# Optimization experiments

Measured on AMD Instinct MI355X. Metric: run time of the kernel, lower is better.

Reference implementation:

```python
import jax, jax.numpy as jnp
import numpy as np

EMBED_DIM = 1024
NUM_HEADS = 16
HEAD_DIM = EMBED_DIM // NUM_HEADS
B, T = 2, 2048


def setup_inputs() -> dict:
    key = jax.random.key(0)
    ks = jax.random.split(key, 9)
    s = 1.0 / np.sqrt(EMBED_DIM)
    return {
        "x": jax.random.normal(ks[0], (B, T, EMBED_DIM), dtype=jnp.float32),
        "W_q": jax.random.uniform(ks[1], (EMBED_DIM, EMBED_DIM), jnp.float32, -s, s),
        "b_q": jax.random.uniform(ks[2], (EMBED_DIM,), jnp.float32, -s, s),
        "W_k": jax.random.uniform(ks[3], (EMBED_DIM, EMBED_DIM), jnp.float32, -s, s),
        "b_k": jax.random.uniform(ks[4], (EMBED_DIM,), jnp.float32, -s, s),
        "W_v": jax.random.uniform(ks[5], (EMBED_DIM, EMBED_DIM), jnp.float32, -s, s),
        "b_v": jax.random.uniform(ks[6], (EMBED_DIM,), jnp.float32, -s, s),
        "W_o": jax.random.uniform(ks[7], (EMBED_DIM, EMBED_DIM), jnp.float32, -s, s),
        "b_o": jax.random.uniform(ks[8], (EMBED_DIM,), jnp.float32, -s, s),
    }


def reference(x, W_q, b_q, W_k, b_k, W_v, b_v, W_o, b_o):
    Bv, Tv, C = x.shape
    # QKV projections (torch Linear: x @ W.T + b); split into heads -> (B,H,T,Dh)
    def proj(W, b):
        return (x @ W.T + b).reshape(Bv, Tv, NUM_HEADS, HEAD_DIM).transpose(0, 2, 1, 3)
    q, k, v = proj(W_q, b_q), proj(W_k, b_k), proj(W_v, b_v)
    scale = 1.0 / np.sqrt(HEAD_DIM).astype(np.float32)
    scores = jnp.einsum("bhqd,bhkd->bhqk", q, k) * scale  # (B,H,T,T)
    causal = jnp.tril(jnp.ones((Tv, Tv), dtype=bool))
    scores = jnp.where(causal, scores, -jnp.inf)
    attn = jax.nn.softmax(scores, axis=-1)
    # dropout is identity in eval / p=0
    out = jnp.einsum("bhqk,bhkd->bhqd", attn, v)  # (B,H,T,Dh)
    out = out.transpose(0, 2, 1, 3).reshape(Bv, Tv, C)
    return out @ W_o.T + b_o
```

## Files before the change

kernel.cpp:

```cpp
#include <hip/hip_runtime.h>
#include <hip/hip_bf16.h>


typedef __bf16 bf16;
typedef __attribute__((ext_vector_type(8))) __bf16 bf16x8;
typedef __attribute__((ext_vector_type(4))) __bf16 bf16x4;
typedef __attribute__((ext_vector_type(4))) float floatx4;

#define LOG2E 1.44269504088896340736f

__device__ __forceinline__ void gl2lds16(const void* g, void* l) {
  __builtin_amdgcn_global_load_lds((const __attribute__((address_space(1))) void*)g,
                                   (__attribute__((address_space(3))) void*)l, 16, 0, 0);
}

__global__ __launch_bounds__(256) void cast_all(
    const float* __restrict__ x, const float* __restrict__ wq,
    const float* __restrict__ wk, const float* __restrict__ wv,
    const float* __restrict__ wo, bf16* __restrict__ dst)
{
  const size_t M1 = (size_t)1 << 20;
  size_t i4 = ((size_t)blockIdx.x * 256 + threadIdx.x) * 4;
  const float* src = x;
  size_t off = i4;
  if (i4 >= 4 * M1) {
    size_t r = i4 - 4 * M1;
    int seg = (int)(r >> 20);
    off = r & (M1 - 1);
    src = (seg == 0) ? wq : (seg == 1) ? wk : (seg == 2) ? wv : wo;
  }
  float4 f = *(const float4*)(src + off);
  bf16x4 o = { (bf16)f.x, (bf16)f.y, (bf16)f.z, (bf16)f.w };
  *(bf16x4*)(dst + i4) = o;
}

template<bool F32OUT, bool QKV, int BN>
__global__ __launch_bounds__(256, 3) void gemm_bt(
    const bf16* __restrict__ A, const bf16* __restrict__ Wb,
    const float* __restrict__ bq, const float* __restrict__ bk,
    const float* __restrict__ bv, void* __restrict__ outb,
    bf16* __restrict__ vt, int M, int N, int K, float qscale)
{
  __shared__ bf16 As[128 * 64];
  __shared__ bf16 Bs[BN * 64];
  const int tid = threadIdx.x;
  const int lane = tid & 63;
  const int wid = tid >> 6;
  const int l15 = lane & 15, l4 = lane >> 4;
  constexpr int I = (BN == 128) ? 4 : 2;
  const int wr = (BN == 128) ? (wid >> 1) : wid;
  const int wc = (BN == 128) ? (wid & 1) : 0;

  const bf16* W;
  const float* bias;
  float osc = 1.0f;
  int n0, mat = 0;
  bf16* outh;
  float* outf;
  if (QKV) {
    mat = blockIdx.x >> 3;
    n0 = (blockIdx.x & 7) << 7;
    W = Wb + ((size_t)mat << 20);
    bias = (mat == 0) ? bq : (mat == 1 ? bk : bv);
    if (mat == 0) osc = qscale;
    outh = (bf16*)outb + ((size_t)mat << 22);
    outf = nullptr;
  } else {
    n0 = blockIdx.x * BN;
    W = Wb;
    bias = bq;
    outf = (float*)outb;
    outh = nullptr;
  }
  const int m0 = blockIdx.y << 7;

  floatx4 acc[I][4] = {};

  for (int k0 = 0; k0 < K; k0 += 64) {
#pragma unroll
    for (int it = 0; it < 4; ++it) {
      int c = it * 256 + tid;
      int row = c >> 3, gs = ((c & 7) ^ (row & 7)) << 3;
      gl2lds16(A + (size_t)(m0 + row) * K + k0 + gs, As + c * 8);
    }
#pragma unroll
    for (int it = 0; it < BN / 32; ++it) {
      int c = it * 256 + tid;
      int row = c >> 3, gs = ((c & 7) ^ (row & 7)) << 3;
      gl2lds16(W + (size_t)(n0 + row) * K + k0 + gs, Bs + c * 8);
    }
    __syncthreads();
#pragma unroll
    for (int kk = 0; kk < 2; ++kk) {
      bf16x8 af[I], bfr[4];
#pragma unroll
      for (int i = 0; i < I; ++i) {
        int r = wr * (I * 16) + i * 16 + l15;
        int g = (kk * 4 + l4) ^ (r & 7);
        af[i] = *(const bf16x8*)(As + r * 64 + g * 8);
      }
#pragma unroll
      for (int j = 0; j < 4; ++j) {
        int r = wc * 64 + j * 16 + l15;
        int g = (kk * 4 + l4) ^ (r & 7);
        bfr[j] = *(const bf16x8*)(Bs + r * 64 + g * 8);
      }
#pragma unroll
      for (int i = 0; i < I; ++i)
#pragma unroll
        for (int j = 0; j < 4; ++j)
          acc[i][j] = __builtin_amdgcn_mfma_f32_16x16x32_bf16(af[i], bfr[j], acc[i][j], 0, 0, 0);
    }
    __syncthreads();
  }

  if (QKV && mat == 2) {
#pragma unroll
    for (int j = 0; j < 4; ++j) {
      int col = n0 + wc * 64 + j * 16 + l15;
      float bv_ = bias[col];
      int h = col >> 6, d = col & 63;
#pragma unroll
      for (int i = 0; i < I; ++i) {
        int row = m0 + wr * (I * 16) + i * 16 + l4 * 4;
        int bb = row >> 11, t = row & 2047;
        bf16x4 pk;
#pragma unroll
        for (int rg = 0; rg < 4; ++rg) pk[rg] = (bf16)(acc[i][j][rg] + bv_);
        *(bf16x4*)(vt + (((size_t)(bb * 16 + h)) << 17) + ((size_t)d << 11) + t) = pk;
      }
    }
    return;
  }

#pragma unroll
  for (int j = 0; j < 4; ++j) {
    int col = n0 + wc * 64 + j * 16 + l15;
    float bv_ = bias[col];
#pragma unroll
    for (int i = 0; i < I; ++i) {
#pragma unroll
      for (int rg = 0; rg < 4; ++rg) {
        int row = m0 + wr * (I * 16) + i * 16 + l4 * 4 + rg;
        float v = (acc[i][j][rg] + bv_) * osc;
        if (F32OUT) outf[(size_t)row * N + col] = v;
        else        outh[(size_t)row * N + col] = (bf16)v;
      }
    }
  }
}

__global__ __launch_bounds__(256, 2) void attn_kernel(
    const bf16* __restrict__ Q, const bf16* __restrict__ Kg,
    const bf16* __restrict__ Vt, bf16* __restrict__ AO)
{
  constexpr int T = 2048, C = 1024;
  __shared__ bf16 Ks[2][64 * 64];
  __shared__ bf16 Vts[2][64 * 64];
  __shared__ bf16 Ps[4][32 * 68];

  const int tid = threadIdx.x;
  const int lane = tid & 63;
  const int w = tid >> 6;
  const int l15 = lane & 15, l4 = lane >> 4;

  const int u = blockIdx.x;
  const int bh = u & 31;
  const int p = u >> 5;
  const int qt = (p < 8) ? (15 - p) : (p - 8);
  const int q0 = qt << 7;
  const int nkt = 2 * qt + 2;
  const size_t base = ((size_t)(bh >> 4) * T) * C + (bh & 15) * 64;
  const bf16* vtb = Vt + ((size_t)bh << 17);

  auto stageK = [&](int j0, int bufi) {
#pragma unroll
    for (int it = 0; it < 2; ++it) {
      int c = it * 256 + tid;
      int row = c >> 3, s = (c & 7) ^ (row & 7);
      gl2lds16(Kg + base + (size_t)(j0 + row) * C + s * 8, &Ks[bufi][c * 8]);
    }
  };
  auto stageV = [&](int j0, int bufi) {
#pragma unroll
    for (int it = 0; it < 2; ++it) {
      int c = it * 256 + tid;
      int row = c >> 3, s = (c & 7) ^ (row & 7);
      gl2lds16(vtb + ((size_t)row << 11) + j0 + s * 8, &Vts[bufi][c * 8]);
    }
  };

  const int qwave = q0 + w * 32;

  bf16x8 qf[2][2];
#pragma unroll
  for (int tq = 0; tq < 2; ++tq) {
    const bf16* qp = Q + base + (size_t)(qwave + tq * 16 + l15) * C + l4 * 8;
    qf[tq][0] = *(const bf16x8*)(qp);
    qf[tq][1] = *(const bf16x8*)(qp + 32);
  }
  floatx4 o[2][4] = {};
  float mrow[2] = {-1e38f, -1e38f};
  float lrow[2] = {0.f, 0.f};

  stageK(0, 0);
  stageV(0, 0);

  for (int jt = 0; jt < nkt; ++jt) {
    __syncthreads();
    const int cur = jt & 1;
    if (jt + 1 < nkt) {
      stageK((jt + 1) << 6, cur ^ 1);
      stageV((jt + 1) << 6, cur ^ 1);
    }
    const int j0 = jt << 6;
    if (j0 > qwave + 31) continue;

    floatx4 s4[4][2] = {};
#pragma unroll
    for (int kk = 0; kk < 2; ++kk) {
      bf16x8 kf[4];
#pragma unroll
      for (int tj = 0; tj < 4; ++tj) {
        int r = tj * 16 + l15;
        int sl = (kk * 4 + l4) ^ (r & 7);
        kf[tj] = *(const bf16x8*)(&Ks[cur][r * 64 + sl * 8]);
      }
#pragma unroll
      for (int tj = 0; tj < 4; ++tj)
#pragma unroll
        for (int tq = 0; tq < 2; ++tq)
          s4[tj][tq] = __builtin_amdgcn_mfma_f32_16x16x32_bf16(kf[tj], qf[tq][kk], s4[tj][tq], 0, 0, 0);
    }

    if (j0 + 63 > qwave) {
#pragma unroll
      for (int tj = 0; tj < 4; ++tj) {
        int j = j0 + tj * 16 + l4 * 4;
#pragma unroll
        for (int tq = 0; tq < 2; ++tq) {
          int q = qwave + tq * 16 + l15;
#pragma unroll
          for (int rg = 0; rg < 4; ++rg)
            if (j + rg > q) s4[tj][tq][rg] = -3e38f;
        }
      }
    }

    float al[2];
#pragma unroll
    for (int tq = 0; tq < 2; ++tq) {
      float mx = -3e38f;
#pragma unroll
      for (int tj = 0; tj < 4; ++tj)
#pragma unroll
        for (int rg = 0; rg < 4; ++rg)
          mx = fmaxf(mx, s4[tj][tq][rg]);
      mx = fmaxf(mx, __shfl_xor(mx, 16, 64));
      mx = fmaxf(mx, __shfl_xor(mx, 32, 64));
      float mnew = fmaxf(mrow[tq], mx);
      al[tq] = __builtin_amdgcn_exp2f(mrow[tq] - mnew);
      mrow[tq] = mnew;
      float psum = 0.f;
#pragma unroll
      for (int tj = 0; tj < 4; ++tj)
#pragma unroll
        for (int rg = 0; rg < 4; ++rg) {
          float e = __builtin_amdgcn_exp2f(s4[tj][tq][rg] - mnew);
          s4[tj][tq][rg] = e;
          psum += e;
        }
      psum += __shfl_xor(psum, 16, 64);
      psum += __shfl_xor(psum, 32, 64);
      lrow[tq] = lrow[tq] * al[tq] + psum;
    }

#pragma unroll
    for (int tq = 0; tq < 2; ++tq)
#pragma unroll
      for (int tj = 0; tj < 4; ++tj) {
        bf16x4 pk = { (bf16)s4[tj][tq][0], (bf16)s4[tj][tq][1],
                      (bf16)s4[tj][tq][2], (bf16)s4[tj][tq][3] };
        *(bf16x4*)(&Ps[w][(tq * 16 + l15) * 68 + tj * 16 + l4 * 4]) = pk;
      }

#pragma unroll
    for (int tq = 0; tq < 2; ++tq)
#pragma unroll
      for (int td = 0; td < 4; ++td)
#pragma unroll
        for (int rg = 0; rg < 4; ++rg)
          o[tq][td][rg] *= al[tq];

#pragma unroll
    for (int tk = 0; tk < 2; ++tk) {
      bf16x8 pf[2];
#pragma unroll
      for (int tq = 0; tq < 2; ++tq)
        pf[tq] = *(const bf16x8*)(&Ps[w][(tq * 16 + l15) * 68 + tk * 32 + l4 * 8]);
#pragma unroll
      for (int td = 0; td < 4; ++td) {
        int r = td * 16 + l15;
        int sl = (tk * 4 + l4) ^ (r & 7);
        bf16x8 vf = *(const bf16x8*)(&Vts[cur][r * 64 + sl * 8]);
#pragma unroll
        for (int tq = 0; tq < 2; ++tq)
          o[tq][td] = __builtin_amdgcn_mfma_f32_16x16x32_bf16(vf, pf[tq], o[tq][td], 0, 0, 0);
      }
    }
  }

#pragma unroll
  for (int tq = 0; tq < 2; ++tq) {
    float inv = 1.0f / lrow[tq];
    int q = qwave + tq * 16 + l15;
#pragma unroll
    for (int td = 0; td < 4; ++td) {
      bf16x4 ok = { (bf16)(o[tq][td][0] * inv), (bf16)(o[tq][td][1] * inv),
                    (bf16)(o[tq][td][2] * inv), (bf16)(o[tq][td][3] * inv) };
      *(bf16x4*)(AO + base + (size_t)q * C + td * 16 + l4 * 4) = ok;
    }
  }
}

extern "C" void kernel_launch(void* const* d_in, const int* in_sizes, int n_in,
                              void* d_out, int out_size, void* d_ws, size_t ws_size,
                              hipStream_t stream) {
  const float* x  = (const float*)d_in[0];
  const float* Wq = (const float*)d_in[1];
  const float* bq = (const float*)d_in[2];
  const float* Wk = (const float*)d_in[3];
  const float* bk = (const float*)d_in[4];
  const float* Wv = (const float*)d_in[5];
  const float* bv = (const float*)d_in[6];
  const float* Wo = (const float*)d_in[7];
  const float* bo = (const float*)d_in[8];

  bf16* ws = (bf16*)d_ws;
  const size_t M1 = (size_t)1 << 20;
  bf16* xb  = ws;
  bf16* wqb = ws + 4 * M1;
  bf16* wob = ws + 7 * M1;
  bf16* Qp  = ws + 8 * M1;
  bf16* Vtp = ws + 16 * M1;
  bf16* AOp = ws + 20 * M1;

  cast_all<<<8192, 256, 0, stream>>>(x, Wq, Wk, Wv, Wo, ws);
  gemm_bt<false, true, 128><<<dim3(24, 32), 256, 0, stream>>>(
      xb, wqb, bq, bk, bv, (void*)Qp, Vtp, 4096, 1024, 1024, 0.125f * LOG2E);
  attn_kernel<<<512, 256, 0, stream>>>(Qp, Qp + 4 * M1, Vtp, AOp);
  gemm_bt<true, false, 64><<<dim3(16, 32), 256, 0, stream>>>(
      AOp, wob, bo, nullptr, nullptr, d_out, nullptr, 4096, 1024, 1024, 1.0f);
}
```

Measured before the change: 187.7 us.

## Restructure attention into single-wave blocks with 16-key steps and register-resident P

The attention kernel now runs one 64-thread wave per block, each owning 32 query rows, with 2048 blocks instead of 512 four-wave blocks. Keys and values are staged in 16-key chunks, and a waitcnt replaces __syncthreads. P stays in registers and feeds a 16x16x16 MFMA directly, so the LDS round trip for probabilities goes away. Rescaling of O is skipped when the row max did not change. The cost is many more loop iterations with small tiles, higher per-step softmax and shuffle overhead, and less K/V reuse across waves, since each wave now loads its own K/V.

```diff
diff --git a/kernel.cpp b/kernel.cpp
--- a/kernel.cpp
+++ b/kernel.cpp
@@ -6,12 +6,27 @@
 typedef __attribute__((ext_vector_type(8))) __bf16 bf16x8;
 typedef __attribute__((ext_vector_type(4))) __bf16 bf16x4;
 typedef __attribute__((ext_vector_type(4))) float floatx4;
+typedef __attribute__((ext_vector_type(4))) short short4v;
 
 #define LOG2E 1.44269504088896340736f
 
 __device__ __forceinline__ void gl2lds16(const void* g, void* l) {
   __builtin_amdgcn_global_load_lds((const __attribute__((address_space(1))) void*)g,
                                    (__attribute__((address_space(3))) void*)l, 16, 0, 0);
+}
+
+__device__ __forceinline__ floatx4 mfma16(bf16x4 a, bf16x4 b, floatx4 c) {
+#if __has_builtin(__builtin_amdgcn_mfma_f32_16x16x16_bf16)
+  return __builtin_amdgcn_mfma_f32_16x16x16_bf16(a, b, c, 0, 0, 0);
+#elif __has_builtin(__builtin_amdgcn_mfma_f32_16x16x16bf16_1k)
+  return __builtin_amdgcn_mfma_f32_16x16x16bf16_1k(
+      __builtin_bit_cast(short4v, a), __builtin_bit_cast(short4v, b), c, 0, 0, 0);
+#else
+  floatx4 d = c;
+  asm volatile("v_mfma_f32_16x16x16_bf16 %0, %1, %2, %0"
+               : "+v"(d) : "v"(a), "v"(b));
+  return d;
+#endif
 }
 
 __global__ __launch_bounds__(256) void cast_all(
@@ -150,55 +165,51 @@
   }
 }
 
-__global__ __launch_bounds__(256, 2) void attn_kernel(
+__global__ __launch_bounds__(64, 4) void attn_kernel(
     const bf16* __restrict__ Q, const bf16* __restrict__ Kg,
     const bf16* __restrict__ Vt, bf16* __restrict__ AO)
 {
   constexpr int T = 2048, C = 1024;
-  __shared__ bf16 Ks[2][64 * 64];
-  __shared__ bf16 Vts[2][64 * 64];
-  __shared__ bf16 Ps[4][32 * 68];
-
-  const int tid = threadIdx.x;
-  const int lane = tid & 63;
-  const int w = tid >> 6;
+  __shared__ bf16 Ks[2][16 * 64];
+  __shared__ bf16 Vts[2][64 * 16];
+
+  const int lane = threadIdx.x;
   const int l15 = lane & 15, l4 = lane >> 4;
 
   const int u = blockIdx.x;
   const int bh = u & 31;
-  const int p = u >> 5;
-  const int qt = (p < 8) ? (15 - p) : (p - 8);
-  const int q0 = qt << 7;
-  const int nkt = 2 * qt + 2;
+  const int qc = 63 - (u >> 5);
+  const int qw = qc << 5;
+  const int ns = 2 * qc + 2;
   const size_t base = ((size_t)(bh >> 4) * T) * C + (bh & 15) * 64;
   const bf16* vtb = Vt + ((size_t)bh << 17);
 
   auto stageK = [&](int j0, int bufi) {
 #pragma unroll
-    for (int it = 0; it < 2; ++it) {
-      int c = it * 256 + tid;
-      int row = c >> 3, s = (c & 7) ^ (row & 7);
-      gl2lds16(Kg + base + (size_t)(j0 + row) * C + s * 8, &Ks[bufi][c * 8]);
+    for (int i = 0; i < 2; ++i) {
+      int c = i * 64 + lane;
+      int row = c >> 3, g = (c & 7) ^ (row & 7);
+      gl2lds16(Kg + base + (size_t)(j0 + row) * C + g * 8, &Ks[bufi][c * 8]);
     }
   };
   auto stageV = [&](int j0, int bufi) {
 #pragma unroll
-    for (int it = 0; it < 2; ++it) {
-      int c = it * 256 + tid;
-      int row = c >> 3, s = (c & 7) ^ (row & 7);
-      gl2lds16(vtb + ((size_t)row << 11) + j0 + s * 8, &Vts[bufi][c * 8]);
+    for (int i = 0; i < 2; ++i) {
+      int c = i * 64 + lane;
+      int d = c >> 1, h = c & 1;
+      int gh = h ^ ((d >> 2) & 1);
+      gl2lds16(vtb + ((size_t)d << 11) + j0 + gh * 8, &Vts[bufi][c * 8]);
     }
   };
 
-  const int qwave = q0 + w * 32;
-
   bf16x8 qf[2][2];
 #pragma unroll
   for (int tq = 0; tq < 2; ++tq) {
-    const bf16* qp = Q + base + (size_t)(qwave + tq * 16 + l15) * C + l4 * 8;
+    const bf16* qp = Q + base + (size_t)(qw + tq * 16 + l15) * C + l4 * 8;
     qf[tq][0] = *(const bf16x8*)(qp);
     qf[tq][1] = *(const bf16x8*)(qp + 32);
   }
+
   floatx4 o[2][4] = {};
   float mrow[2] = {-1e38f, -1e38f};
   float lrow[2] = {0.f, 0.f};
@@ -206,114 +217,95 @@
   stageK(0, 0);
   stageV(0, 0);
 
-  for (int jt = 0; jt < nkt; ++jt) {
-    __syncthreads();
-    const int cur = jt & 1;
-    if (jt + 1 < nkt) {
-      stageK((jt + 1) << 6, cur ^ 1);
-      stageV((jt + 1) << 6, cur ^ 1);
-    }
-    const int j0 = jt << 6;
-    if (j0 > qwave + 31) continue;
-
-    floatx4 s4[4][2] = {};
+  int buf = 0;
+  for (int s = 0; s < ns; ++s) {
+    __builtin_amdgcn_sched_barrier(0);
+    const bool more = (s + 1 < ns);
+    if (more) {
+      stageK((s + 1) << 4, buf ^ 1);
+      stageV((s + 1) << 4, buf ^ 1);
+      __builtin_amdgcn_s_waitcnt(0x0F74);
+    } else {
+      __builtin_amdgcn_s_waitcnt(0x0F70);
+    }
+    __builtin_amdgcn_sched_barrier(0);
+
+    const int j0 = s << 4;
+
+    floatx4 s4[2] = {};
 #pragma unroll
     for (int kk = 0; kk < 2; ++kk) {
-      bf16x8 kf[4];
-#pragma unroll
-      for (int tj = 0; tj < 4; ++tj) {
-        int r = tj * 16 + l15;
-        int sl = (kk * 4 + l4) ^ (r & 7);
-        kf[tj] = *(const bf16x8*)(&Ks[cur][r * 64 + sl * 8]);
-      }
-#pragma unroll
-      for (int tj = 0; tj < 4; ++tj)
-#pragma unroll
-        for (int tq = 0; tq < 2; ++tq)
-          s4[tj][tq] = __builtin_amdgcn_mfma_f32_16x16x32_bf16(kf[tj], qf[tq][kk], s4[tj][tq], 0, 0, 0);
-    }
-
-    if (j0 + 63 > qwave) {
-#pragma unroll
-      for (int tj = 0; tj < 4; ++tj) {
-        int j = j0 + tj * 16 + l4 * 4;
-#pragma unroll
-        for (int tq = 0; tq < 2; ++tq) {
-          int q = qwave + tq * 16 + l15;
-#pragma unroll
-          for (int rg = 0; rg < 4; ++rg)
-            if (j + rg > q) s4[tj][tq][rg] = -3e38f;
-        }
+      bf16x8 kf = *(const bf16x8*)(&Ks[buf][l15 * 64 + (((kk * 4 + l4) ^ (l15 & 7)) * 8)]);
+      s4[0] = __builtin_amdgcn_mfma_f32_16x16x32_bf16(kf, qf[0][kk], s4[0], 0, 0, 0);
+      s4[1] = __builtin_amdgcn_mfma_f32_16x16x32_bf16(kf, qf[1][kk], s4[1], 0, 0, 0);
+    }
+
+    if (j0 + 15 > qw) {
+      int j = j0 + l4 * 4;
+#pragma unroll
+      for (int tq = 0; tq < 2; ++tq) {
+        int q = qw + tq * 16 + l15;
+#pragma unroll
+        for (int rg = 0; rg < 4; ++rg)
+          if (j + rg > q) s4[tq][rg] = -3e38f;
       }
     }
 
     float al[2];
 #pragma unroll
     for (int tq = 0; tq < 2; ++tq) {
-      float mx = -3e38f;
-#pragma unroll
-      for (int tj = 0; tj < 4; ++tj)
-#pragma unroll
-        for (int rg = 0; rg < 4; ++rg)
-          mx = fmaxf(mx, s4[tj][tq][rg]);
+      float mx = fmaxf(fmaxf(s4[tq][0], s4[tq][1]), fmaxf(s4[tq][2], s4[tq][3]));
       mx = fmaxf(mx, __shfl_xor(mx, 16, 64));
       mx = fmaxf(mx, __shfl_xor(mx, 32, 64));
       float mnew = fmaxf(mrow[tq], mx);
       al[tq] = __builtin_amdgcn_exp2f(mrow[tq] - mnew);
       mrow[tq] = mnew;
-      float psum = 0.f;
-#pragma unroll
-      for (int tj = 0; tj < 4; ++tj)
-#pragma unroll
-        for (int rg = 0; rg < 4; ++rg) {
-          float e = __builtin_amdgcn_exp2f(s4[tj][tq][rg] - mnew);
-          s4[tj][tq][rg] = e;
-          psum += e;
-        }
-      psum += __shfl_xor(psum, 16, 64);
-      psum += __shfl_xor(psum, 32, 64);
-      lrow[tq] = lrow[tq] * al[tq] + psum;
-    }
-
-#pragma unroll
-    for (int tq = 0; tq < 2; ++tq)
-#pragma unroll
-      for (int tj = 0; tj < 4; ++tj) {
-        bf16x4 pk = { (bf16)s4[tj][tq][0], (bf16)s4[tj][tq][1],
-                      (bf16)s4[tj][tq][2], (bf16)s4[tj][tq][3] };
-        *(bf16x4*)(&Ps[w][(tq * 16 + l15) * 68 + tj * 16 + l4 * 4]) = pk;
-      }
-
-#pragma unroll
-    for (int tq = 0; tq < 2; ++tq)
-#pragma unroll
-      for (int td = 0; td < 4; ++td)
-#pragma unroll
-        for (int rg = 0; rg < 4; ++rg)
-          o[tq][td][rg] *= al[tq];
-
-#pragma unroll
-    for (int tk = 0; tk < 2; ++tk) {
-      bf16x8 pf[2];
+      float ps = 0.f;
+#pragma unroll
+      for (int rg = 0; rg < 4; ++rg) {
+        float e = __builtin_amdgcn_exp2f(s4[tq][rg] - mnew);
+        s4[tq][rg] = e;
+        ps += e;
+      }
+      ps += __shfl_xor(ps, 16, 64);
+      ps += __shfl_xor(ps, 32, 64);
+      lrow[tq] = lrow[tq] * al[tq] + ps;
+    }
+
+    if (!__all((al[0] == 1.f) & (al[1] == 1.f))) {
 #pragma unroll
       for (int tq = 0; tq < 2; ++tq)
-        pf[tq] = *(const bf16x8*)(&Ps[w][(tq * 16 + l15) * 68 + tk * 32 + l4 * 8]);
-#pragma unroll
-      for (int td = 0; td < 4; ++td) {
-        int r = td * 16 + l15;
-        int sl = (tk * 4 + l4) ^ (r & 7);
-        bf16x8 vf = *(const bf16x8*)(&Vts[cur][r * 64 + sl * 8]);
-#pragma unroll
-        for (int tq = 0; tq < 2; ++tq)
-          o[tq][td] = __builtin_amdgcn_mfma_f32_16x16x32_bf16(vf, pf[tq], o[tq][td], 0, 0, 0);
-      }
-    }
+#pragma unroll
+        for (int td = 0; td < 4; ++td)
+#pragma unroll
+          for (int rg = 0; rg < 4; ++rg)
+            o[tq][td][rg] *= al[tq];
+    }
+
+    bf16x4 pf[2];
+#pragma unroll
+    for (int tq = 0; tq < 2; ++tq) {
+      bf16x4 pk = { (bf16)s4[tq][0], (bf16)s4[tq][1],
+                    (bf16)s4[tq][2], (bf16)s4[tq][3] };
+      pf[tq] = pk;
+    }
+
+#pragma unroll
+    for (int td = 0; td < 4; ++td) {
+      int d = td * 16 + l15;
+      int uu = ((l4 >> 1) ^ ((d >> 2) & 1)) * 2 + (l4 & 1);
+      bf16x4 vf = *(const bf16x4*)(&Vts[buf][d * 16 + uu * 4]);
+      o[0][td] = mfma16(vf, pf[0], o[0][td]);
+      o[1][td] = mfma16(vf, pf[1], o[1][td]);
+    }
+
+    buf ^= 1;
   }
 
 #pragma unroll
   for (int tq = 0; tq < 2; ++tq) {
     float inv = 1.0f / lrow[tq];
-    int q = qwave + tq * 16 + l15;
+    int q = qw + tq * 16 + l15;
 #pragma unroll
     for (int td = 0; td < 4; ++td) {
       bf16x4 ok = { (bf16)(o[tq][td][0] * inv), (bf16)(o[tq][td][1] * inv),
@@ -348,7 +340,7 @@
   cast_all<<<8192, 256, 0, stream>>>(x, Wq, Wk, Wv, Wo, ws);
   gemm_bt<false, true, 128><<<dim3(24, 32), 256, 0, stream>>>(
       xb, wqb, bq, bk, bv, (void*)Qp, Vtp, 4096, 1024, 1024, 0.125f * LOG2E);
-  attn_kernel<<<512, 256, 0, stream>>>(Qp, Qp + 4 * M1, Vtp, AOp);
+  attn_kernel<<<2048, 64, 0, stream>>>(Qp, Qp + 4 * M1, Vtp, AOp);
   gemm_bt<true, false, 64><<<dim3(16, 32), 256, 0, stream>>>(
       AOp, wob, bo, nullptr, nullptr, d_out, nullptr, 4096, 1024, 1024, 1.0f);
 }
```

Result: slower. 246.9 us (+31.6%).

## Keep softmax probabilities in registers and permute V^T layout to match

Applied to the files above, without the earlier changes.

The P tile no longer takes a round trip through LDS; the exp'd scores are packed to bf16 in registers and fed straight into 16x16x16 MFMAs. The V projection epilogue writes V^T with a permuted time index so the V fragments line up with the register layout of P. The rescale of the output accumulator is skipped when every lane's alpha equals one. In exchange, the PV product runs at twice as many MFMA instructions with half the K each, and the layout change couples the projection kernel to the attention kernel.

```diff
diff --git a/kernel.cpp b/kernel.cpp
--- a/kernel.cpp
+++ b/kernel.cpp
@@ -6,12 +6,27 @@
 typedef __attribute__((ext_vector_type(8))) __bf16 bf16x8;
 typedef __attribute__((ext_vector_type(4))) __bf16 bf16x4;
 typedef __attribute__((ext_vector_type(4))) float floatx4;
+typedef __attribute__((ext_vector_type(4))) short short4v;
 
 #define LOG2E 1.44269504088896340736f
 
 __device__ __forceinline__ void gl2lds16(const void* g, void* l) {
   __builtin_amdgcn_global_load_lds((const __attribute__((address_space(1))) void*)g,
                                    (__attribute__((address_space(3))) void*)l, 16, 0, 0);
+}
+
+__device__ __forceinline__ floatx4 mfma16(bf16x4 a, bf16x4 b, floatx4 c) {
+#if __has_builtin(__builtin_amdgcn_mfma_f32_16x16x16_bf16)
+  return __builtin_amdgcn_mfma_f32_16x16x16_bf16(a, b, c, 0, 0, 0);
+#elif __has_builtin(__builtin_amdgcn_mfma_f32_16x16x16bf16_1k)
+  return __builtin_amdgcn_mfma_f32_16x16x16bf16_1k(
+      __builtin_bit_cast(short4v, a), __builtin_bit_cast(short4v, b), c, 0, 0, 0);
+#else
+  floatx4 d = c;
+  asm volatile("v_mfma_f32_16x16x16_bf16 %0, %1, %2, %0"
+               : "+v"(d) : "v"(a), "v"(b));
+  return d;
+#endif
 }
 
 __global__ __launch_bounds__(256) void cast_all(
@@ -124,10 +139,11 @@
       for (int i = 0; i < I; ++i) {
         int row = m0 + wr * (I * 16) + i * 16 + l4 * 4;
         int bb = row >> 11, t = row & 2047;
+        int tp = (t & ~31) | (((t >> 2) & 3) << 3) | (((t >> 4) & 1) << 2);
         bf16x4 pk;
 #pragma unroll
         for (int rg = 0; rg < 4; ++rg) pk[rg] = (bf16)(acc[i][j][rg] + bv_);
-        *(bf16x4*)(vt + (((size_t)(bb * 16 + h)) << 17) + ((size_t)d << 11) + t) = pk;
+        *(bf16x4*)(vt + (((size_t)(bb * 16 + h)) << 17) + ((size_t)d << 11) + tp) = pk;
       }
     }
     return;
@@ -157,7 +173,6 @@
   constexpr int T = 2048, C = 1024;
   __shared__ bf16 Ks[2][64 * 64];
   __shared__ bf16 Vts[2][64 * 64];
-  __shared__ bf16 Ps[4][32 * 68];
 
   const int tid = threadIdx.x;
   const int lane = tid & 63;
@@ -177,16 +192,16 @@
 #pragma unroll
     for (int it = 0; it < 2; ++it) {
       int c = it * 256 + tid;
-      int row = c >> 3, s = (c & 7) ^ (row & 7);
-      gl2lds16(Kg + base + (size_t)(j0 + row) * C + s * 8, &Ks[bufi][c * 8]);
+      int row = c >> 3, g = (c & 7) ^ (row & 7);
+      gl2lds16(Kg + base + (size_t)(j0 + row) * C + g * 8, &Ks[bufi][c * 8]);
     }
   };
   auto stageV = [&](int j0, int bufi) {
 #pragma unroll
     for (int it = 0; it < 2; ++it) {
       int c = it * 256 + tid;
-      int row = c >> 3, s = (c & 7) ^ (row & 7);
-      gl2lds16(vtb + ((size_t)row << 11) + j0 + s * 8, &Vts[bufi][c * 8]);
+      int d = c >> 3, g = (c & 7) ^ (d & 7);
+      gl2lds16(vtb + ((size_t)d << 11) + j0 + g * 8, &Vts[bufi][c * 8]);
     }
   };
 
@@ -199,6 +214,7 @@
     qf[tq][0] = *(const bf16x8*)(qp);
     qf[tq][1] = *(const bf16x8*)(qp + 32);
   }
+
   floatx4 o[2][4] = {};
   float mrow[2] = {-1e38f, -1e38f};
   float lrow[2] = {0.f, 0.f};
@@ -219,18 +235,14 @@
     floatx4 s4[4][2] = {};
 #pragma unroll
     for (int kk = 0; kk < 2; ++kk) {
-      bf16x8 kf[4];
 #pragma unroll
       for (int tj = 0; tj < 4; ++tj) {
         int r = tj * 16 + l15;
-        int sl = (kk * 4 + l4) ^ (r & 7);
-        kf[tj] = *(const bf16x8*)(&Ks[cur][r * 64 + sl * 8]);
-      }
-#pragma unroll
-      for (int tj = 0; tj < 4; ++tj)
-#pragma unroll
-        for (int tq = 0; tq < 2; ++tq)
-          s4[tj][tq] = __builtin_amdgcn_mfma_f32_16x16x32_bf16(kf[tj], qf[tq][kk], s4[tj][tq], 0, 0, 0);
+        int g = (kk * 4 + l4) ^ (r & 7);
+        bf16x8 kf = *(const bf16x8*)(&Ks[cur][r * 64 + g * 8]);
+        s4[tj][0] = __builtin_amdgcn_mfma_f32_16x16x32_bf16(kf, qf[0][kk], s4[tj][0], 0, 0, 0);
+        s4[tj][1] = __builtin_amdgcn_mfma_f32_16x16x32_bf16(kf, qf[1][kk], s4[tj][1], 0, 0, 0);
+      }
     }
 
     if (j0 + 63 > qwave) {
@@ -261,51 +273,53 @@
       float mnew = fmaxf(mrow[tq], mx);
       al[tq] = __builtin_amdgcn_exp2f(mrow[tq] - mnew);
       mrow[tq] = mnew;
-      float psum = 0.f;
+      float ps = 0.f;
 #pragma unroll
       for (int tj = 0; tj < 4; ++tj)
 #pragma unroll
         for (int rg = 0; rg < 4; ++rg) {
           float e = __builtin_amdgcn_exp2f(s4[tj][tq][rg] - mnew);
           s4[tj][tq][rg] = e;
-          psum += e;
+          ps += e;
         }
-      psum += __shfl_xor(psum, 16, 64);
-      psum += __shfl_xor(psum, 32, 64);
-      lrow[tq] = lrow[tq] * al[tq] + psum;
-    }
-
-#pragma unroll
-    for (int tq = 0; tq < 2; ++tq)
-#pragma unroll
-      for (int tj = 0; tj < 4; ++tj) {
+      ps += __shfl_xor(ps, 16, 64);
+      ps += __shfl_xor(ps, 32, 64);
+      lrow[tq] = lrow[tq] * al[tq] + ps;
+    }
+
+    if (!__all((al[0] == 1.f) & (al[1] == 1.f))) {
+#pragma unroll
+      for (int tq = 0; tq < 2; ++tq)
+#pragma unroll
+        for (int td = 0; td < 4; ++td)
+#pragma unroll
+          for (int rg = 0; rg < 4; ++rg)
+            o[tq][td][rg] *= al[tq];
+    }
+
+    bf16x4 pf[4][2];
+#pragma unroll
+    for (int tj = 0; tj < 4; ++tj)
+#pragma unroll
+      for (int tq = 0; tq < 2; ++tq) {
         bf16x4 pk = { (bf16)s4[tj][tq][0], (bf16)s4[tj][tq][1],
                       (bf16)s4[tj][tq][2], (bf16)s4[tj][tq][3] };
-        *(bf16x4*)(&Ps[w][(tq * 16 + l15) * 68 + tj * 16 + l4 * 4]) = pk;
-      }
-
-#pragma unroll
-    for (int tq = 0; tq < 2; ++tq)
-#pragma unroll
-      for (int td = 0; td < 4; ++td)
-#pragma unroll
-        for (int rg = 0; rg < 4; ++rg)
-          o[tq][td][rg] *= al[tq];
+        pf[tj][tq] = pk;
+      }
 
 #pragma unroll
     for (int tk = 0; tk < 2; ++tk) {
-      bf16x8 pf[2];
-#pragma unroll
-      for (int tq = 0; tq < 2; ++tq)
-        pf[tq] = *(const bf16x8*)(&Ps[w][(tq * 16 + l15) * 68 + tk * 32 + l4 * 8]);
 #pragma unroll
       for (int td = 0; td < 4; ++td) {
         int r = td * 16 + l15;
-        int sl = (tk * 4 + l4) ^ (r & 7);
-        bf16x8 vf = *(const bf16x8*)(&Vts[cur][r * 64 + sl * 8]);
-#pragma unroll
-        for (int tq = 0; tq < 2; ++tq)
-          o[tq][td] = __builtin_amdgcn_mfma_f32_16x16x32_bf16(vf, pf[tq], o[tq][td], 0, 0, 0);
+        int g = (tk * 4 + l4) ^ (r & 7);
+        bf16x8 vf = *(const bf16x8*)(&Vts[cur][r * 64 + g * 8]);
+        bf16x4 lo = { vf[0], vf[1], vf[2], vf[3] };
+        bf16x4 hi = { vf[4], vf[5], vf[6], vf[7] };
+        o[0][td] = mfma16(lo, pf[tk * 2][0], o[0][td]);
+        o[0][td] = mfma16(hi, pf[tk * 2 + 1][0], o[0][td]);
+        o[1][td] = mfma16(lo, pf[tk * 2][1], o[1][td]);
+        o[1][td] = mfma16(hi, pf[tk * 2 + 1][1], o[1][td]);
       }
     }
   }
```

Measured after the change: 189.8 us. About the same (+1.1%).
